# Optimization experiments

Measured on AMD Instinct MI355X. Metric: run time of the kernel, lower is better.

Reference implementation:

```python
import jax, jax.numpy as jnp
import numpy as np

VOCAB, EMBED, HIDDEN, OUT = 1024, 512, 1024, 1024
B, T = 1024, 32


def setup_inputs() -> dict:
    key = jax.random.key(0)
    ks = jax.random.split(key, 10)
    s_emb = 1.0 / np.sqrt(VOCAB)
    s_ih = 1.0 / np.sqrt(HIDDEN)  # PyTorch RNNCell init scale uses hidden_size
    s_out = 1.0 / np.sqrt(HIDDEN)
    return {
        "message": jax.random.normal(ks[0], (B, T, VOCAB), dtype=jnp.float32),
        "W_emb": jax.random.uniform(ks[1], (EMBED, VOCAB), jnp.float32, -s_emb, s_emb),
        "b_emb": jax.random.uniform(ks[2], (EMBED,), jnp.float32, -s_emb, s_emb),
        "W_ih": jax.random.uniform(ks[3], (HIDDEN, EMBED), jnp.float32, -s_ih, s_ih),
        "b_ih": jax.random.uniform(ks[4], (HIDDEN,), jnp.float32, -s_ih, s_ih),
        "W_hh": jax.random.uniform(ks[5], (HIDDEN, HIDDEN), jnp.float32, -s_ih, s_ih),
        "b_hh": jax.random.uniform(ks[6], (HIDDEN,), jnp.float32, -s_ih, s_ih),
        "W_out": jax.random.uniform(ks[7], (OUT, HIDDEN), jnp.float32, -s_out, s_out),
        "b_out": jax.random.uniform(ks[8], (OUT,), jnp.float32, -s_out, s_out),
    }


def reference(message, W_emb, b_emb, W_ih, b_ih, W_hh, b_hh, W_out, b_out):
    # emb: [B, T, E] -- Linear embedding of (relaxed one-hot) message
    emb = jnp.einsum("btv,ev->bte", message, W_emb) + b_emb
    # Precompute input projections for all steps at once: [T, B, H]
    x_proj = jnp.einsum("bte,he->tbh", emb, W_ih) + b_ih

    def step(h, x_t):
        h_new = jnp.tanh(x_t + h @ W_hh.T + b_hh)
        return h_new, None

    h0 = jnp.zeros((message.shape[0], W_hh.shape[0]), dtype=message.dtype)
    h_T, _ = jax.lax.scan(step, h0, x_proj)
    out = h_T @ W_out.T + b_out  # [B, OUT]
    return out  # agent is identity here
```

## Files before the change

### kernel.cpp

```cpp
#include <hip/hip_runtime.h>
#include <cstdint>
#include <cstddef>

#define B_DIM 1024
#define T_DIM 32
#define V_DIM 1024
#define E_DIM 512
#define H_DIM 1024
#define O_DIM 1024

typedef unsigned short u16;
typedef __attribute__((ext_vector_type(8))) __bf16 bf16x8;
typedef __attribute__((ext_vector_type(4))) float f32x4;

__device__ __forceinline__ float bf2f(u16 u) {
  union { unsigned int i; float f; } v; v.i = ((unsigned int)u) << 16; return v.f;
}
__device__ __forceinline__ u16 f2bf(float f) {
  union { float f; unsigned int i; } v; v.f = f;
  return (u16)((v.i + 0x7fffu + ((v.i >> 16) & 1u)) >> 16);
}
__device__ __forceinline__ void async_cp16(const void* g, void* l) {
  __builtin_amdgcn_global_load_lds(
      (const __attribute__((address_space(1))) void*)g,
      (__attribute__((address_space(3))) void*)l, 16, 0, 0);
}
__device__ __forceinline__ float fast_tanh(float v) {
  return 1.f - 2.f / (__expf(2.f * v) + 1.f);
}

__global__ __launch_bounds__(256) void convert_all(
    const float* __restrict__ Whh, const float* __restrict__ Wout,
    const float* __restrict__ msg, u16* __restrict__ dWhh,
    u16* __restrict__ dWout, u16* __restrict__ dmsg) {
  const int QW = 262144;
  const int QM = 8388608;
  const int total = dmsg ? (2 * QW + QM) : (2 * QW);
  int i = blockIdx.x * 256 + threadIdx.x;
  const int stride = gridDim.x * 256;
  for (; i < total; i += stride) {
    const float4* src; ushort4* dst; int j;
    if (i < QW)            { src = (const float4*)Whh;  dst = (ushort4*)dWhh;  j = i; }
    else if (i < 2 * QW)   { src = (const float4*)Wout; dst = (ushort4*)dWout; j = i - QW; }
    else                   { src = (const float4*)msg;  dst = (ushort4*)dmsg;  j = i - 2 * QW; }
    float4 v = src[j];
    ushort4 o = {f2bf(v.x), f2bf(v.y), f2bf(v.z), f2bf(v.w)};
    dst[j] = o;
  }
}

__global__ __launch_bounds__(256) void wcomb_valu(
    const float* __restrict__ Wih, const float* __restrict__ Wemb,
    u16* __restrict__ Wc) {
  __shared__ __align__(16) float As[16][68];
  __shared__ __align__(16) float Bs[16][68];
  const int tx = threadIdx.x & 15, ty = threadIdx.x >> 4;
  const int v0 = blockIdx.x * 64, h0 = blockIdx.y * 64;
  float acc[4][4] = {};
  for (int kt = 0; kt < 32; ++kt) {
#pragma unroll
    for (int i = 0; i < 4; ++i) {
      int idx = threadIdx.x + i * 256;
      int row = idx >> 4, k = idx & 15;
      As[k][row] = Wih[(size_t)(h0 + row) * E_DIM + kt * 16 + k];
      Bs[k][row] = Wemb[(size_t)(kt * 16 + k) * V_DIM + v0 + row];
    }
    __syncthreads();
    for (int k = 0; k < 16; ++k) {
      float4 a = *(const float4*)&As[k][ty * 4];
      float4 b = *(const float4*)&Bs[k][tx * 4];
      const float av[4] = {a.x, a.y, a.z, a.w}, bv[4] = {b.x, b.y, b.z, b.w};
#pragma unroll
      for (int i = 0; i < 4; ++i)
#pragma unroll
        for (int j = 0; j < 4; ++j) acc[i][j] += av[i] * bv[j];
    }
    __syncthreads();
  }
#pragma unroll
  for (int i = 0; i < 4; ++i)
#pragma unroll
    for (int j = 0; j < 4; ++j)
      Wc[(size_t)(h0 + ty * 4 + i) * V_DIM + v0 + tx * 4 + j] = f2bf(acc[i][j]);
}

__global__ __launch_bounds__(256) void bcomb_valu(
    const float* __restrict__ Wih, const float* __restrict__ bemb,
    const float* __restrict__ bih, float* __restrict__ bc) {
  int h = blockIdx.x * 256 + threadIdx.x;
  float s = 0.f;
  for (int e = 0; e < E_DIM; ++e) s += Wih[(size_t)h * E_DIM + e] * bemb[e];
  bc[h] = s + bih[h];
}

template <int MODE>
__global__ __launch_bounds__(256) void gemm_bt(
    const u16* __restrict__ A, const u16* __restrict__ Bm,
    const u16* __restrict__ x, const float* __restrict__ bias,
    void* __restrict__ outp) {
  constexpr int LDSE = 49152;
  __shared__ __align__(16) u16 lds[LDSE];
  const int tid = threadIdx.x, lane = tid & 63, w = tid >> 6;
  const int lrow = lane >> 4, lcol = lane & 15;
  const int l7 = lane & 7, r8 = lane >> 3;
  const int p = blockIdx.x;
  int mt, nt;
  {
    int xk = p & 7, q = p >> 3;
    mt = xk * 32 + (q >> 3);
    nt = q & 7;
  }
  const int m0 = mt * 128, n0 = nt * 128;
  const int mq = (w & 1) * 64, nq = (w >> 1) * 64;
  const int half = w >> 1, wv = w & 1;

  auto stage = [&](int kk, int d) {
    const u16* src = half ? Bm : A;
    const int rbase = half ? n0 : m0;
#pragma unroll
    for (int i = 0; i < 8; ++i) {
      int row = wv * 64 + i * 8 + r8;
      async_cp16(src + (size_t)(rbase + row) * H_DIM + kk * 64 + ((l7 ^ r8) << 3),
                 lds + d * 16384 + half * 8192 + (wv * 64 + i * 8) * 64);
    }
  };

  f32x4 acc[4][4] = {};
  auto kchunk = [&](int d) {
    const u16* base = lds + d * 16384;
#pragma unroll
    for (int ks = 0; ks < 2; ++ks) {
      const int ce = ks * 32 + lrow * 8;
      bf16x8 a[4], b[4];
#pragma unroll
      for (int i = 0; i < 4; ++i) {
        int row = mq + i * 16 + lcol;
        a[i] = *(const bf16x8*)(base + row * 64 + (ce ^ ((row & 7) << 3)));
      }
#pragma unroll
      for (int i = 0; i < 4; ++i) {
        int row = nq + i * 16 + lcol;
        b[i] = *(const bf16x8*)(base + 8192 + row * 64 + (ce ^ ((row & 7) << 3)));
      }
#pragma unroll
      for (int i = 0; i < 4; ++i)
#pragma unroll
        for (int j = 0; j < 4; ++j)
          acc[i][j] = __builtin_amdgcn_mfma_f32_16x16x32_bf16(a[i], b[j], acc[i][j], 0, 0, 0);
    }
  };

  stage(0, 0); stage(1, 1); stage(2, 2);
#pragma unroll
  for (int kk = 0; kk < 16; ++kk) {
    if (kk <= 13)      asm volatile("s_waitcnt vmcnt(16)" ::: "memory");
    else if (kk == 14) asm volatile("s_waitcnt vmcnt(8)" ::: "memory");
    else               asm volatile("s_waitcnt vmcnt(0)" ::: "memory");
    __builtin_amdgcn_s_barrier();
    kchunk(kk % 3);
    __builtin_amdgcn_s_barrier();
    if (kk <= 12) stage(kk + 3, kk % 3);
  }

  float bv[4];
#pragma unroll
  for (int j = 0; j < 4; ++j) bv[j] = bias[n0 + nq + j * 16 + lcol];
#pragma unroll
  for (int i = 0; i < 4; ++i)
#pragma unroll
    for (int rr = 0; rr < 4; ++rr) {
      int rg = m0 + mq + i * 16 + lrow * 4 + rr;
      int bI = rg >> 5, tI = rg & 31;
      u16* dst = (u16*)outp + ((size_t)tI * B_DIM + bI) * H_DIM + n0 + nq;
#pragma unroll
      for (int j = 0; j < 4; ++j)
        dst[j * 16 + lcol] = f2bf(acc[i][j][rr] + bv[j]);
    }
}

template <int MODE>
__global__ __launch_bounds__(256) void step64(
    const u16* __restrict__ A, const u16* __restrict__ Bm,
    const u16* __restrict__ x, const float* __restrict__ bias,
    void* __restrict__ outp) {
  constexpr int XOFF = 24576;
  constexpr int LDSE = (MODE == 1) ? 28672 : 24576;
  __shared__ __align__(16) u16 lds[LDSE];
  const int tid = threadIdx.x, lane = tid & 63, w = tid >> 6;
  const int lrow = lane >> 4, lcol = lane & 15;
  const int l7 = lane & 7, r8 = lane >> 3;
  const int p = blockIdx.x;
  const int xcd = p & 7, q = p >> 3;
  const int mt = xcd * 2 + (q >> 4), nt = q & 15;
  const int m0 = mt * 64, n0 = nt * 64;
  const int mq = (w & 1) * 32, nq = (w >> 1) * 32;
  const int half = w >> 1, wv = w & 1;

  auto stage = [&](int kk, int d) {
    const u16* src = half ? Bm : A;
    const int rbase = half ? n0 : m0;
#pragma unroll
    for (int i = 0; i < 4; ++i) {
      int row = wv * 32 + i * 8 + r8;
      async_cp16(src + (size_t)(rbase + row) * H_DIM + kk * 64 + ((l7 ^ r8) << 3),
                 lds + d * 8192 + half * 4096 + (wv * 32 + i * 8) * 64);
    }
  };
  auto stage_x = [&]() {
#pragma unroll
    for (int i = 0; i < 2; ++i)
      async_cp16(x + (size_t)(m0 + i * 32 + w * 8 + r8) * H_DIM + n0 + l7 * 8,
                 lds + XOFF + (i * 32 + w * 8) * 64);
  };

  f32x4 acc[2][2] = {};
  auto kchunk = [&](int d) {
    const u16* base = lds + d * 8192;
#pragma unroll
    for (int ks = 0; ks < 2; ++ks) {
      const int ce = ks * 32 + lrow * 8;
      bf16x8 a[2], b[2];
#pragma unroll
      for (int i = 0; i < 2; ++i) {
        int row = mq + i * 16 + lcol;
        a[i] = *(const bf16x8*)(base + row * 64 + (ce ^ ((row & 7) << 3)));
      }
#pragma unroll
      for (int j = 0; j < 2; ++j) {
        int row = nq + j * 16 + lcol;
        b[j] = *(const bf16x8*)(base + 4096 + row * 64 + (ce ^ ((row & 7) << 3)));
      }
#pragma unroll
      for (int i = 0; i < 2; ++i)
#pragma unroll
        for (int j = 0; j < 2; ++j)
          acc[i][j] = __builtin_amdgcn_mfma_f32_16x16x32_bf16(a[i], b[j], acc[i][j], 0, 0, 0);
    }
  };

  if (A != nullptr) {
    if (MODE == 1) stage_x();
    stage(0, 0); stage(1, 1); stage(2, 2);
#pragma unroll
    for (int kk = 0; kk < 16; ++kk) {
      if (kk <= 13)      asm volatile("s_waitcnt vmcnt(8)" ::: "memory");
      else if (kk == 14) asm volatile("s_waitcnt vmcnt(4)" ::: "memory");
      else               asm volatile("s_waitcnt vmcnt(0)" ::: "memory");
      __builtin_amdgcn_s_barrier();
      kchunk(kk % 3);
      __builtin_amdgcn_s_barrier();
      if (kk <= 12) stage(kk + 3, kk % 3);
    }
  } else {
    if (MODE == 1) stage_x();
    asm volatile("s_waitcnt vmcnt(0)" ::: "memory");
    __builtin_amdgcn_s_barrier();
  }

  float bv[2] = {bias[n0 + nq + lcol], bias[n0 + nq + 16 + lcol]};
  if (MODE == 2) {
#pragma unroll
    for (int i = 0; i < 2; ++i)
#pragma unroll
      for (int rr = 0; rr < 4; ++rr) {
        int row = m0 + mq + i * 16 + lrow * 4 + rr;
#pragma unroll
        for (int j = 0; j < 2; ++j)
          ((float*)outp)[(size_t)row * O_DIM + n0 + nq + j * 16 + lcol] =
              acc[i][j][rr] + bv[j];
      }
  } else {
#pragma unroll
    for (int i = 0; i < 2; ++i)
#pragma unroll
      for (int rr = 0; rr < 4; ++rr) {
        int rowl = mq + i * 16 + lrow * 4 + rr;
#pragma unroll
        for (int j = 0; j < 2; ++j) {
          int col = nq + j * 16 + lcol;
          float v = acc[i][j][rr] + bv[j] + bf2f(lds[XOFF + rowl * 64 + col]);
          lds[rowl * 64 + col] = f2bf(fast_tanh(v));
        }
      }
    __syncthreads();
    {
      int row = tid >> 2, c = (tid & 3) * 16;
      const uint4* s = (const uint4*)(lds + row * 64 + c);
      uint4 v0 = s[0], v1 = s[1];
      uint4* g = (uint4*)((u16*)outp + (size_t)(m0 + row) * H_DIM + n0 + c);
      g[0] = v0;
      g[1] = v1;
    }
  }
}

__global__ __launch_bounds__(256) void xproj_mfma(
    const float* __restrict__ msg, const u16* __restrict__ Wc,
    const float* __restrict__ bc, u16* __restrict__ xp) {
  __shared__ u16 As[128 * 64];
  __shared__ u16 Bs[128 * 64];
  const int tid = threadIdx.x, lane = tid & 63, w = tid >> 6;
  const int lrow = lane >> 4, lcol = lane & 15;
  const int p = blockIdx.y * gridDim.x + blockIdx.x;
  const int xk = p & 7, q = p >> 3;
  const int m0 = (xk * 32 + (q >> 3)) * 128;
  const int n0 = (q & 7) * 128;
  const int mq = (w & 1) * 64, nq = (w >> 1) * 64;
  f32x4 acc[4][4] = {};
  const int r8 = lane >> 3, l7 = lane & 7;
  const int ar = tid >> 1, ak = (tid & 1) * 32;

  auto stageB = [&](int kk) {
#pragma unroll
    for (int i = 0; i < 4; ++i) {
      int ch = w * 4 + i;
      async_cp16(Wc + (size_t)(n0 + ch * 8 + r8) * V_DIM + kk * 64 + ((l7 ^ r8) << 3),
                 Bs + ch * 512);
    }
  };
  float4 areg[8];
  auto loadA = [&](int kk) {
    const float4* src = (const float4*)(msg + (size_t)(m0 + ar) * V_DIM + kk * 64 + ak);
#pragma unroll
    for (int i = 0; i < 8; ++i) areg[i] = src[i];
  };
  auto writeA = [&]() {
    u16 tmp[32];
#pragma unroll
    for (int i = 0; i < 8; ++i) {
      tmp[i * 4 + 0] = f2bf(areg[i].x);
      tmp[i * 4 + 1] = f2bf(areg[i].y);
      tmp[i * 4 + 2] = f2bf(areg[i].z);
      tmp[i * 4 + 3] = f2bf(areg[i].w);
    }
#pragma unroll
    for (int i = 0; i < 4; ++i) {
      int c = (ak + i * 8) ^ ((ar & 7) << 3);
      *(uint4*)(As + (size_t)ar * 64 + c) = *(const uint4*)(tmp + i * 8);
    }
  };

  loadA(0);
  stageB(0);
  writeA();
  for (int kk = 0; kk < 16; ++kk) {
    __syncthreads();
    if (kk < 15) loadA(kk + 1);
#pragma unroll
    for (int ks = 0; ks < 2; ++ks) {
      const int kb = ks * 32 + lrow * 8;
      bf16x8 a[4], b[4];
#pragma unroll
      for (int i = 0; i < 4; ++i) {
        int row = mq + i * 16 + lcol;
        a[i] = *(const bf16x8*)(As + row * 64 + (kb ^ ((row & 7) << 3)));
      }
#pragma unroll
      for (int i = 0; i < 4; ++i) {
        int row = nq + i * 16 + lcol;
        b[i] = *(const bf16x8*)(Bs + row * 64 + (kb ^ ((row & 7) << 3)));
      }
#pragma unroll
      for (int i = 0; i < 4; ++i)
#pragma unroll
        for (int j = 0; j < 4; ++j)
          acc[i][j] = __builtin_amdgcn_mfma_f32_16x16x32_bf16(a[i], b[j], acc[i][j], 0, 0, 0);
    }
    __syncthreads();
    if (kk < 15) { stageB(kk + 1); writeA(); }
  }
  float bcv[4];
#pragma unroll
  for (int j = 0; j < 4; ++j) bcv[j] = bc[n0 + nq + j * 16 + lcol];
#pragma unroll
  for (int i = 0; i < 4; ++i)
#pragma unroll
    for (int rr = 0; rr < 4; ++rr) {
      int rg = m0 + mq + i * 16 + lrow * 4 + rr;
      int bI = rg >> 5, tI = rg & 31;
      u16* dst = xp + ((size_t)tI * B_DIM + bI) * H_DIM + n0 + nq;
#pragma unroll
      for (int j = 0; j < 4; ++j)
        dst[j * 16 + lcol] = f2bf(acc[i][j][rr] + bcv[j]);
    }
}

extern "C" void kernel_launch(void* const* d_in, const int* in_sizes, int n_in,
                              void* d_out, int out_size, void* d_ws, size_t ws_size,
                              hipStream_t stream) {
  const float* msg  = (const float*)d_in[0];
  const float* Wemb = (const float*)d_in[1];
  const float* bemb = (const float*)d_in[2];
  const float* Wih  = (const float*)d_in[3];
  const float* bih  = (const float*)d_in[4];
  const float* Whh  = (const float*)d_in[5];
  const float* bhh  = (const float*)d_in[6];
  const float* Wout = (const float*)d_in[7];
  const float* bout = (const float*)d_in[8];
  char* ws = (char*)d_ws;

  float* bc   = (float*)ws;
  u16* Wc     = (u16*)(ws + 4096);
  u16* Whh_b  = (u16*)(ws + 2101248);
  u16* Wout_b = (u16*)(ws + 4198400);
  u16* hA     = (u16*)(ws + 6295552);
  u16* hB     = (u16*)(ws + 8392704);
  u16* xp     = (u16*)(ws + 10489856);
  u16* msgb   = (u16*)(ws + 77598720);
  const size_t NEED_SMALL = 77598720;
  const size_t NEED_BIG   = 77598720 + 67108864;
  if (ws_size < NEED_SMALL) return;
  const bool big = ws_size >= NEED_BIG;

  if (big) {
    convert_all<<<2048, 256, 0, stream>>>(Whh, Wout, msg, Whh_b, Wout_b, msgb);
  } else {
    convert_all<<<512, 256, 0, stream>>>(Whh, Wout, nullptr, Whh_b, Wout_b, nullptr);
  }
  wcomb_valu<<<dim3(16, 16), 256, 0, stream>>>(Wih, Wemb, Wc);
  bcomb_valu<<<4, 256, 0, stream>>>(Wih, bemb, bih, bc);

  if (big) {
    gemm_bt<0><<<2048, 256, 0, stream>>>(msgb, Wc, nullptr, bc, xp);
  } else {
    xproj_mfma<<<dim3(8, 256), 256, 0, stream>>>(msg, Wc, bc, xp);
  }

  step64<1><<<256, 256, 0, stream>>>(nullptr, Whh_b, xp, bhh, hA);
  for (int t = 1; t < 32; ++t) {
    const u16* hin = (t & 1) ? hA : hB;
    u16* hout = (t & 1) ? hB : hA;
    step64<1><<<256, 256, 0, stream>>>(hin, Whh_b,
                                       xp + (size_t)t * B_DIM * H_DIM, bhh, hout);
  }
  step64<2><<<256, 256, 0, stream>>>(hB, Wout_b, nullptr, bout, d_out);
}
```

Measured before the change: 566.9 us.

## Replace per-step RNN launches with cooperative kernels using grid-wide atomic barriers

The 32 per-timestep kernel launches become 4 cooperative launches, each running 8 recurrence steps with a grid-wide spin barrier on an atomic counter between steps. Hidden states are written in place over the consumed xp slot, using coherent (sc0 sc1) loads and stores so other blocks see them. The aim is to remove per-launch overhead and tail gaps between steps. The cost is atomic spin-wait synchronization, and correctness depends on all 256 blocks being co-resident.

```diff
diff --git a/kernel.cpp b/kernel.cpp
--- a/kernel.cpp
+++ b/kernel.cpp
@@ -12,6 +12,7 @@
 typedef unsigned short u16;
 typedef __attribute__((ext_vector_type(8))) __bf16 bf16x8;
 typedef __attribute__((ext_vector_type(4))) float f32x4;
+typedef __attribute__((ext_vector_type(4))) unsigned int u32x4;
 
 __device__ __forceinline__ float bf2f(u16 u) {
   union { unsigned int i; float f; } v; v.i = ((unsigned int)u) << 16; return v.f;
@@ -86,30 +87,25 @@
 
 __global__ __launch_bounds__(256) void bcomb_valu(
     const float* __restrict__ Wih, const float* __restrict__ bemb,
-    const float* __restrict__ bih, float* __restrict__ bc) {
+    const float* __restrict__ bih, float* __restrict__ bc,
+    unsigned* __restrict__ ctr) {
+  if (blockIdx.x == 0 && threadIdx.x == 0) *ctr = 0;
   int h = blockIdx.x * 256 + threadIdx.x;
   float s = 0.f;
   for (int e = 0; e < E_DIM; ++e) s += Wih[(size_t)h * E_DIM + e] * bemb[e];
   bc[h] = s + bih[h];
 }
 
-template <int MODE>
-__global__ __launch_bounds__(256) void gemm_bt(
+__global__ __launch_bounds__(256) void gemm_xp(
     const u16* __restrict__ A, const u16* __restrict__ Bm,
-    const u16* __restrict__ x, const float* __restrict__ bias,
-    void* __restrict__ outp) {
-  constexpr int LDSE = 49152;
-  __shared__ __align__(16) u16 lds[LDSE];
+    const float* __restrict__ bias, u16* __restrict__ outp) {
+  __shared__ __align__(16) u16 lds[49152];
   const int tid = threadIdx.x, lane = tid & 63, w = tid >> 6;
   const int lrow = lane >> 4, lcol = lane & 15;
   const int l7 = lane & 7, r8 = lane >> 3;
   const int p = blockIdx.x;
-  int mt, nt;
-  {
-    int xk = p & 7, q = p >> 3;
-    mt = xk * 32 + (q >> 3);
-    nt = q & 7;
-  }
+  const int xk = p & 7, q = p >> 3;
+  const int mt = xk * 32 + (q >> 3), nt = q & 7;
   const int m0 = mt * 128, n0 = nt * 128;
   const int mq = (w & 1) * 64, nq = (w >> 1) * 64;
   const int half = w >> 1, wv = w & 1;
@@ -171,21 +167,17 @@
     for (int rr = 0; rr < 4; ++rr) {
       int rg = m0 + mq + i * 16 + lrow * 4 + rr;
       int bI = rg >> 5, tI = rg & 31;
-      u16* dst = (u16*)outp + ((size_t)tI * B_DIM + bI) * H_DIM + n0 + nq;
+      u16* dst = outp + ((size_t)tI * B_DIM + bI) * H_DIM + n0 + nq;
 #pragma unroll
       for (int j = 0; j < 4; ++j)
         dst[j * 16 + lcol] = f2bf(acc[i][j][rr] + bv[j]);
     }
 }
 
-template <int MODE>
-__global__ __launch_bounds__(256) void step64(
-    const u16* __restrict__ A, const u16* __restrict__ Bm,
-    const u16* __restrict__ x, const float* __restrict__ bias,
-    void* __restrict__ outp) {
-  constexpr int XOFF = 24576;
-  constexpr int LDSE = (MODE == 1) ? 28672 : 24576;
-  __shared__ __align__(16) u16 lds[LDSE];
+__global__ __launch_bounds__(256) void steps8(
+    const u16* __restrict__ Bm, u16* __restrict__ xp,
+    const float* __restrict__ bhh, unsigned* __restrict__ ctr, int t0) {
+  __shared__ __align__(16) u16 lds[24576];
   const int tid = threadIdx.x, lane = tid & 63, w = tid >> 6;
   const int lrow = lane >> 4, lcol = lane & 15;
   const int l7 = lane & 7, r8 = lane >> 3;
@@ -195,6 +187,128 @@
   const int m0 = mt * 64, n0 = nt * 64;
   const int mq = (w & 1) * 32, nq = (w >> 1) * 32;
   const int half = w >> 1, wv = w & 1;
+  const float bv0 = bhh[n0 + nq + lcol], bv1 = bhh[n0 + nq + 16 + lcol];
+  const int xrow = tid >> 2, xce = (tid & 3) * 16;
+
+  for (int s = 0; s < 8; ++s) {
+    const int t = t0 + s;
+    u16* slot = xp + (size_t)t * (B_DIM * H_DIM);
+    const u16* A = (t == 0) ? nullptr : xp + (size_t)(t - 1) * (B_DIM * H_DIM);
+
+    const u16* xgp = slot + (size_t)(m0 + xrow) * H_DIM + n0 + xce;
+    u32x4 xv0, xv1;
+    asm volatile(
+        "global_load_dwordx4 %0, %2, off sc0 sc1\n\t"
+        "global_load_dwordx4 %1, %3, off sc0 sc1"
+        : "=v"(xv0), "=v"(xv1)
+        : "v"(xgp), "v"(xgp + 8)
+        : "memory");
+
+    f32x4 acc[2][2] = {};
+    if (A != nullptr) {
+      auto stage = [&](int kk, int d) {
+        const u16* src = half ? Bm : A;
+        const int rbase = half ? n0 : m0;
+#pragma unroll
+        for (int i = 0; i < 4; ++i) {
+          int row = wv * 32 + i * 8 + r8;
+          async_cp16(src + (size_t)(rbase + row) * H_DIM + kk * 64 + ((l7 ^ r8) << 3),
+                     lds + d * 8192 + half * 4096 + (wv * 32 + i * 8) * 64);
+        }
+      };
+      stage(0, 0); stage(1, 1); stage(2, 2);
+#pragma unroll
+      for (int kk = 0; kk < 16; ++kk) {
+        if (kk <= 13)      asm volatile("s_waitcnt vmcnt(8)" ::: "memory");
+        else if (kk == 14) asm volatile("s_waitcnt vmcnt(4)" ::: "memory");
+        else               asm volatile("s_waitcnt vmcnt(0)" ::: "memory");
+        __builtin_amdgcn_s_barrier();
+        {
+          const u16* base = lds + (kk % 3) * 8192;
+#pragma unroll
+          for (int ks = 0; ks < 2; ++ks) {
+            const int ce = ks * 32 + lrow * 8;
+            bf16x8 a0, a1, b0, b1;
+            {
+              int rA0 = mq + lcol, rA1 = mq + 16 + lcol;
+              int rB0 = nq + lcol, rB1 = nq + 16 + lcol;
+              a0 = *(const bf16x8*)(base + rA0 * 64 + (ce ^ ((rA0 & 7) << 3)));
+              a1 = *(const bf16x8*)(base + rA1 * 64 + (ce ^ ((rA1 & 7) << 3)));
+              b0 = *(const bf16x8*)(base + 4096 + rB0 * 64 + (ce ^ ((rB0 & 7) << 3)));
+              b1 = *(const bf16x8*)(base + 4096 + rB1 * 64 + (ce ^ ((rB1 & 7) << 3)));
+            }
+            acc[0][0] = __builtin_amdgcn_mfma_f32_16x16x32_bf16(a0, b0, acc[0][0], 0, 0, 0);
+            acc[0][1] = __builtin_amdgcn_mfma_f32_16x16x32_bf16(a0, b1, acc[0][1], 0, 0, 0);
+            acc[1][0] = __builtin_amdgcn_mfma_f32_16x16x32_bf16(a1, b0, acc[1][0], 0, 0, 0);
+            acc[1][1] = __builtin_amdgcn_mfma_f32_16x16x32_bf16(a1, b1, acc[1][1], 0, 0, 0);
+          }
+        }
+        __builtin_amdgcn_s_barrier();
+        if (kk <= 12) stage(kk + 3, kk % 3);
+      }
+    } else {
+      asm volatile("s_waitcnt vmcnt(0)" ::: "memory");
+      __builtin_amdgcn_s_barrier();
+    }
+
+    *(u32x4*)(lds + 8192 + xrow * 64 + xce) = xv0;
+    *(u32x4*)(lds + 8192 + xrow * 64 + xce + 8) = xv1;
+    __syncthreads();
+#pragma unroll
+    for (int i = 0; i < 2; ++i)
+#pragma unroll
+      for (int rr = 0; rr < 4; ++rr) {
+        int rowl = mq + i * 16 + lrow * 4 + rr;
+#pragma unroll
+        for (int j = 0; j < 2; ++j) {
+          int col = nq + j * 16 + lcol;
+          float v = acc[i][j][rr] + (j ? bv1 : bv0) + bf2f(lds[8192 + rowl * 64 + col]);
+          lds[rowl * 64 + col] = f2bf(fast_tanh(v));
+        }
+      }
+    __syncthreads();
+    {
+      const u32x4* sp = (const u32x4*)(lds + xrow * 64 + xce);
+      u32x4 h0 = sp[0], h1 = sp[1];
+      u16* gp = slot + (size_t)(m0 + xrow) * H_DIM + n0 + xce;
+      if (s < 7) {
+        asm volatile(
+            "global_store_dwordx4 %0, %2, off sc0 sc1\n\t"
+            "global_store_dwordx4 %1, %3, off sc0 sc1"
+            :: "v"(gp), "v"(gp + 8), "v"(h0), "v"(h1)
+            : "memory");
+        asm volatile("s_waitcnt vmcnt(0)" ::: "memory");
+        __syncthreads();
+        if (tid == 0) {
+          const unsigned tgt = 256u * (unsigned)(7 * (t0 >> 3) + s + 1);
+          __hip_atomic_fetch_add(ctr, 1u, __ATOMIC_RELAXED,
+                                 __HIP_MEMORY_SCOPE_AGENT);
+          while (__hip_atomic_load(ctr, __ATOMIC_RELAXED,
+                                   __HIP_MEMORY_SCOPE_AGENT) < tgt)
+            __builtin_amdgcn_s_sleep(4);
+        }
+        __syncthreads();
+      } else {
+        *(u32x4*)gp = h0;
+        *(u32x4*)(gp + 8) = h1;
+      }
+    }
+  }
+}
+
+__global__ __launch_bounds__(256) void out_gemm(
+    const u16* __restrict__ A, const u16* __restrict__ Bm,
+    const float* __restrict__ bias, float* __restrict__ outp) {
+  __shared__ __align__(16) u16 lds[24576];
+  const int tid = threadIdx.x, lane = tid & 63, w = tid >> 6;
+  const int lrow = lane >> 4, lcol = lane & 15;
+  const int l7 = lane & 7, r8 = lane >> 3;
+  const int p = blockIdx.x;
+  const int xcd = p & 7, q = p >> 3;
+  const int mt = xcd * 2 + (q >> 4), nt = q & 15;
+  const int m0 = mt * 64, n0 = nt * 64;
+  const int mq = (w & 1) * 32, nq = (w >> 1) * 32;
+  const int half = w >> 1, wv = w & 1;
 
   auto stage = [&](int kk, int d) {
     const u16* src = half ? Bm : A;
@@ -206,92 +320,46 @@
                  lds + d * 8192 + half * 4096 + (wv * 32 + i * 8) * 64);
     }
   };
-  auto stage_x = [&]() {
-#pragma unroll
-    for (int i = 0; i < 2; ++i)
-      async_cp16(x + (size_t)(m0 + i * 32 + w * 8 + r8) * H_DIM + n0 + l7 * 8,
-                 lds + XOFF + (i * 32 + w * 8) * 64);
-  };
-
   f32x4 acc[2][2] = {};
   auto kchunk = [&](int d) {
     const u16* base = lds + d * 8192;
 #pragma unroll
     for (int ks = 0; ks < 2; ++ks) {
       const int ce = ks * 32 + lrow * 8;
-      bf16x8 a[2], b[2];
-#pragma unroll
-      for (int i = 0; i < 2; ++i) {
-        int row = mq + i * 16 + lcol;
-        a[i] = *(const bf16x8*)(base + row * 64 + (ce ^ ((row & 7) << 3)));
-      }
-#pragma unroll
-      for (int j = 0; j < 2; ++j) {
-        int row = nq + j * 16 + lcol;
-        b[j] = *(const bf16x8*)(base + 4096 + row * 64 + (ce ^ ((row & 7) << 3)));
-      }
-#pragma unroll
-      for (int i = 0; i < 2; ++i)
-#pragma unroll
-        for (int j = 0; j < 2; ++j)
-          acc[i][j] = __builtin_amdgcn_mfma_f32_16x16x32_bf16(a[i], b[j], acc[i][j], 0, 0, 0);
-    }
-  };
-
-  if (A != nullptr) {
-    if (MODE == 1) stage_x();
-    stage(0, 0); stage(1, 1); stage(2, 2);
-#pragma unroll
-    for (int kk = 0; kk < 16; ++kk) {
-      if (kk <= 13)      asm volatile("s_waitcnt vmcnt(8)" ::: "memory");
-      else if (kk == 14) asm volatile("s_waitcnt vmcnt(4)" ::: "memory");
-      else               asm volatile("s_waitcnt vmcnt(0)" ::: "memory");
-      __builtin_amdgcn_s_barrier();
-      kchunk(kk % 3);
-      __builtin_amdgcn_s_barrier();
-      if (kk <= 12) stage(kk + 3, kk % 3);
-    }
-  } else {
-    if (MODE == 1) stage_x();
-    asm volatile("s_waitcnt vmcnt(0)" ::: "memory");
+      int rA0 = mq + lcol, rA1 = mq + 16 + lcol;
+      int rB0 = nq + lcol, rB1 = nq + 16 + lcol;
+      bf16x8 a0 = *(const bf16x8*)(base + rA0 * 64 + (ce ^ ((rA0 & 7) << 3)));
+      bf16x8 a1 = *(const bf16x8*)(base + rA1 * 64 + (ce ^ ((rA1 & 7) << 3)));
+      bf16x8 b0 = *(const bf16x8*)(base + 4096 + rB0 * 64 + (ce ^ ((rB0 & 7) << 3)));
+      bf16x8 b1 = *(const bf16x8*)(base + 4096 + rB1 * 64 + (ce ^ ((rB1 & 7) << 3)));
+      acc[0][0] = __builtin_amdgcn_mfma_f32_16x16x32_bf16(a0, b0, acc[0][0], 0, 0, 0);
+      acc[0][1] = __builtin_amdgcn_mfma_f32_16x16x32_bf16(a0, b1, acc[0][1], 0, 0, 0);
+      acc[1][0] = __builtin_amdgcn_mfma_f32_16x16x32_bf16(a1, b0, acc[1][0], 0, 0, 0);
+      acc[1][1] = __builtin_amdgcn_mfma_f32_16x16x32_bf16(a1, b1, acc[1][1], 0, 0, 0);
+    }
+  };
+  stage(0, 0); stage(1, 1); stage(2, 2);
+#pragma unroll
+  for (int kk = 0; kk < 16; ++kk) {
+    if (kk <= 13)      asm volatile("s_waitcnt vmcnt(8)" ::: "memory");
+    else if (kk == 14) asm volatile("s_waitcnt vmcnt(4)" ::: "memory");
+    else               asm volatile("s_waitcnt vmcnt(0)" ::: "memory");
     __builtin_amdgcn_s_barrier();
-  }
-
+    kchunk(kk % 3);
+    __builtin_amdgcn_s_barrier();
+    if (kk <= 12) stage(kk + 3, kk % 3);
+  }
   float bv[2] = {bias[n0 + nq + lcol], bias[n0 + nq + 16 + lcol]};
-  if (MODE == 2) {
-#pragma unroll
-    for (int i = 0; i < 2; ++i)
-#pragma unroll
-      for (int rr = 0; rr < 4; ++rr) {
-        int row = m0 + mq + i * 16 + lrow * 4 + rr;
-#pragma unroll
-        for (int j = 0; j < 2; ++j)
-          ((float*)outp)[(size_t)row * O_DIM + n0 + nq + j * 16 + lcol] =
-              acc[i][j][rr] + bv[j];
-      }
-  } else {
-#pragma unroll
-    for (int i = 0; i < 2; ++i)
-#pragma unroll
-      for (int rr = 0; rr < 4; ++rr) {
-        int rowl = mq + i * 16 + lrow * 4 + rr;
-#pragma unroll
-        for (int j = 0; j < 2; ++j) {
-          int col = nq + j * 16 + lcol;
-          float v = acc[i][j][rr] + bv[j] + bf2f(lds[XOFF + rowl * 64 + col]);
-          lds[rowl * 64 + col] = f2bf(fast_tanh(v));
-        }
-      }
-    __syncthreads();
-    {
-      int row = tid >> 2, c = (tid & 3) * 16;
-      const uint4* s = (const uint4*)(lds + row * 64 + c);
-      uint4 v0 = s[0], v1 = s[1];
-      uint4* g = (uint4*)((u16*)outp + (size_t)(m0 + row) * H_DIM + n0 + c);
-      g[0] = v0;
-      g[1] = v1;
-    }
-  }
+#pragma unroll
+  for (int i = 0; i < 2; ++i)
+#pragma unroll
+    for (int rr = 0; rr < 4; ++rr) {
+      int row = m0 + mq + i * 16 + lrow * 4 + rr;
+#pragma unroll
+      for (int j = 0; j < 2; ++j)
+        outp[(size_t)row * O_DIM + n0 + nq + j * 16 + lcol] =
+            acc[i][j][rr] + bv[j];
+    }
 }
 
 __global__ __launch_bounds__(256) void xproj_mfma(
@@ -399,14 +467,13 @@
   const float* bout = (const float*)d_in[8];
   char* ws = (char*)d_ws;
 
-  float* bc   = (float*)ws;
-  u16* Wc     = (u16*)(ws + 4096);
-  u16* Whh_b  = (u16*)(ws + 2101248);
-  u16* Wout_b = (u16*)(ws + 4198400);
-  u16* hA     = (u16*)(ws + 6295552);
-  u16* hB     = (u16*)(ws + 8392704);
-  u16* xp     = (u16*)(ws + 10489856);
-  u16* msgb   = (u16*)(ws + 77598720);
+  float* bc     = (float*)ws;
+  u16* Wc       = (u16*)(ws + 4096);
+  u16* Whh_b    = (u16*)(ws + 2101248);
+  u16* Wout_b   = (u16*)(ws + 4198400);
+  unsigned* ctr = (unsigned*)(ws + 6295552);
+  u16* xp       = (u16*)(ws + 10489856);
+  u16* msgb     = (u16*)(ws + 77598720);
   const size_t NEED_SMALL = 77598720;
   const size_t NEED_BIG   = 77598720 + 67108864;
   if (ws_size < NEED_SMALL) return;
@@ -418,20 +485,22 @@
     convert_all<<<512, 256, 0, stream>>>(Whh, Wout, nullptr, Whh_b, Wout_b, nullptr);
   }
   wcomb_valu<<<dim3(16, 16), 256, 0, stream>>>(Wih, Wemb, Wc);
-  bcomb_valu<<<4, 256, 0, stream>>>(Wih, bemb, bih, bc);
+  bcomb_valu<<<4, 256, 0, stream>>>(Wih, bemb, bih, bc, ctr);
 
   if (big) {
-    gemm_bt<0><<<2048, 256, 0, stream>>>(msgb, Wc, nullptr, bc, xp);
+    gemm_xp<<<2048, 256, 0, stream>>>(msgb, Wc, bc, xp);
   } else {
     xproj_mfma<<<dim3(8, 256), 256, 0, stream>>>(msg, Wc, bc, xp);
   }
 
-  step64<1><<<256, 256, 0, stream>>>(nullptr, Whh_b, xp, bhh, hA);
-  for (int t = 1; t < 32; ++t) {
-    const u16* hin = (t & 1) ? hA : hB;
-    u16* hout = (t & 1) ? hB : hA;
-    step64<1><<<256, 256, 0, stream>>>(hin, Whh_b,
-                                       xp + (size_t)t * B_DIM * H_DIM, bhh, hout);
-  }
-  step64<2><<<256, 256, 0, stream>>>(hB, Wout_b, nullptr, bout, d_out);
-}
+  for (int c = 0; c < 4; ++c) {
+    const u16* a_w = Whh_b; u16* a_xp = xp; const float* a_b = bhh;
+    unsigned* a_c = ctr; int a_t0 = c * 8;
+    void* kargs[] = {(void*)&a_w, (void*)&a_xp, (void*)&a_b,
+                     (void*)&a_c, (void*)&a_t0};
+    (void)hipLaunchCooperativeKernel((const void*)steps8, dim3(256), dim3(256),
+                                     kargs, 0, stream);
+  }
+  out_gemm<<<256, 256, 0, stream>>>(xp + (size_t)31 * B_DIM * H_DIM, Wout_b,
+                                    bout, (float*)d_out);
+}
```

Result: slower. 773.8 us (+36.5%).

## Fuse prep kernels, fold first RNN step into xproj GEMM, double-buffer

Applied to the files above, without the earlier changes.

Merges the weight conversion, combined-weight GEMM and combined-bias kernels into one launch that dispatches on block index. The x-projection GEMM epilogue now applies tanh with b_hh for t=0, since h0 is zero, which removes one recurrent step launch. The GEMM's LDS pipeline drops from triple to double buffering, which cuts LDS use but gives less latency hiding. The fused prep kernel puts light and heavy work under a single grid, and the first step now writes its h output into the xp buffer.

```diff
diff --git a/kernel.cpp b/kernel.cpp
--- a/kernel.cpp
+++ b/kernel.cpp
@@ -29,87 +29,80 @@
   return 1.f - 2.f / (__expf(2.f * v) + 1.f);
 }
 
-__global__ __launch_bounds__(256) void convert_all(
+__global__ __launch_bounds__(256) void prep_all(
     const float* __restrict__ Whh, const float* __restrict__ Wout,
-    const float* __restrict__ msg, u16* __restrict__ dWhh,
-    u16* __restrict__ dWout, u16* __restrict__ dmsg) {
-  const int QW = 262144;
-  const int QM = 8388608;
-  const int total = dmsg ? (2 * QW + QM) : (2 * QW);
-  int i = blockIdx.x * 256 + threadIdx.x;
-  const int stride = gridDim.x * 256;
-  for (; i < total; i += stride) {
-    const float4* src; ushort4* dst; int j;
-    if (i < QW)            { src = (const float4*)Whh;  dst = (ushort4*)dWhh;  j = i; }
-    else if (i < 2 * QW)   { src = (const float4*)Wout; dst = (ushort4*)dWout; j = i - QW; }
-    else                   { src = (const float4*)msg;  dst = (ushort4*)dmsg;  j = i - 2 * QW; }
-    float4 v = src[j];
-    ushort4 o = {f2bf(v.x), f2bf(v.y), f2bf(v.z), f2bf(v.w)};
-    dst[j] = o;
-  }
-}
-
-__global__ __launch_bounds__(256) void wcomb_valu(
-    const float* __restrict__ Wih, const float* __restrict__ Wemb,
-    u16* __restrict__ Wc) {
+    const float* __restrict__ msg, const float* __restrict__ Wih,
+    const float* __restrict__ Wemb, const float* __restrict__ bemb,
+    const float* __restrict__ bih, u16* __restrict__ dWhh,
+    u16* __restrict__ dWout, u16* __restrict__ dmsg,
+    u16* __restrict__ Wc, float* __restrict__ bc) {
   __shared__ __align__(16) float As[16][68];
   __shared__ __align__(16) float Bs[16][68];
-  const int tx = threadIdx.x & 15, ty = threadIdx.x >> 4;
-  const int v0 = blockIdx.x * 64, h0 = blockIdx.y * 64;
-  float acc[4][4] = {};
-  for (int kt = 0; kt < 32; ++kt) {
-#pragma unroll
-    for (int i = 0; i < 4; ++i) {
-      int idx = threadIdx.x + i * 256;
-      int row = idx >> 4, k = idx & 15;
-      As[k][row] = Wih[(size_t)(h0 + row) * E_DIM + kt * 16 + k];
-      Bs[k][row] = Wemb[(size_t)(kt * 16 + k) * V_DIM + v0 + row];
-    }
-    __syncthreads();
-    for (int k = 0; k < 16; ++k) {
-      float4 a = *(const float4*)&As[k][ty * 4];
-      float4 b = *(const float4*)&Bs[k][tx * 4];
-      const float av[4] = {a.x, a.y, a.z, a.w}, bv[4] = {b.x, b.y, b.z, b.w};
-#pragma unroll
-      for (int i = 0; i < 4; ++i)
-#pragma unroll
-        for (int j = 0; j < 4; ++j) acc[i][j] += av[i] * bv[j];
-    }
-    __syncthreads();
-  }
-#pragma unroll
-  for (int i = 0; i < 4; ++i)
-#pragma unroll
-    for (int j = 0; j < 4; ++j)
-      Wc[(size_t)(h0 + ty * 4 + i) * V_DIM + v0 + tx * 4 + j] = f2bf(acc[i][j]);
-}
-
-__global__ __launch_bounds__(256) void bcomb_valu(
-    const float* __restrict__ Wih, const float* __restrict__ bemb,
-    const float* __restrict__ bih, float* __restrict__ bc) {
-  int h = blockIdx.x * 256 + threadIdx.x;
-  float s = 0.f;
-  for (int e = 0; e < E_DIM; ++e) s += Wih[(size_t)h * E_DIM + e] * bemb[e];
-  bc[h] = s + bih[h];
-}
-
-template <int MODE>
-__global__ __launch_bounds__(256) void gemm_bt(
+  const int bid = blockIdx.x;
+  if (bid < 2048) {
+    const int QW = 262144;
+    const int QM = 8388608;
+    const int total = dmsg ? (2 * QW + QM) : (2 * QW);
+    int i = bid * 256 + threadIdx.x;
+    const int stride = 2048 * 256;
+    for (; i < total; i += stride) {
+      const float4* src; ushort4* dst; int j;
+      if (i < QW)          { src = (const float4*)Whh;  dst = (ushort4*)dWhh;  j = i; }
+      else if (i < 2 * QW) { src = (const float4*)Wout; dst = (ushort4*)dWout; j = i - QW; }
+      else                 { src = (const float4*)msg;  dst = (ushort4*)dmsg;  j = i - 2 * QW; }
+      float4 v = src[j];
+      ushort4 o = {f2bf(v.x), f2bf(v.y), f2bf(v.z), f2bf(v.w)};
+      dst[j] = o;
+    }
+  } else if (bid < 2304) {
+    const int b2 = bid - 2048;
+    const int tx = threadIdx.x & 15, ty = threadIdx.x >> 4;
+    const int v0 = (b2 & 15) * 64, h0 = (b2 >> 4) * 64;
+    float acc[4][4] = {};
+    for (int kt = 0; kt < 32; ++kt) {
+#pragma unroll
+      for (int i = 0; i < 4; ++i) {
+        int idx = threadIdx.x + i * 256;
+        int row = idx >> 4, k = idx & 15;
+        As[k][row] = Wih[(size_t)(h0 + row) * E_DIM + kt * 16 + k];
+        Bs[k][row] = Wemb[(size_t)(kt * 16 + k) * V_DIM + v0 + row];
+      }
+      __syncthreads();
+      for (int k = 0; k < 16; ++k) {
+        float4 a = *(const float4*)&As[k][ty * 4];
+        float4 b = *(const float4*)&Bs[k][tx * 4];
+        const float av[4] = {a.x, a.y, a.z, a.w}, bv[4] = {b.x, b.y, b.z, b.w};
+#pragma unroll
+        for (int i = 0; i < 4; ++i)
+#pragma unroll
+          for (int j = 0; j < 4; ++j) acc[i][j] += av[i] * bv[j];
+      }
+      __syncthreads();
+    }
+#pragma unroll
+    for (int i = 0; i < 4; ++i)
+#pragma unroll
+      for (int j = 0; j < 4; ++j)
+        Wc[(size_t)(h0 + ty * 4 + i) * V_DIM + v0 + tx * 4 + j] = f2bf(acc[i][j]);
+  } else {
+    int h = (bid - 2304) * 256 + threadIdx.x;
+    float s = 0.f;
+    for (int e = 0; e < E_DIM; ++e) s += Wih[(size_t)h * E_DIM + e] * bemb[e];
+    bc[h] = s + bih[h];
+  }
+}
+
+__global__ __launch_bounds__(256) void gemm_xp(
     const u16* __restrict__ A, const u16* __restrict__ Bm,
-    const u16* __restrict__ x, const float* __restrict__ bias,
-    void* __restrict__ outp) {
-  constexpr int LDSE = 49152;
-  __shared__ __align__(16) u16 lds[LDSE];
+    const float* __restrict__ bias, const float* __restrict__ bhh,
+    u16* __restrict__ outp) {
+  __shared__ __align__(16) u16 lds[32768];
   const int tid = threadIdx.x, lane = tid & 63, w = tid >> 6;
   const int lrow = lane >> 4, lcol = lane & 15;
   const int l7 = lane & 7, r8 = lane >> 3;
   const int p = blockIdx.x;
-  int mt, nt;
-  {
-    int xk = p & 7, q = p >> 3;
-    mt = xk * 32 + (q >> 3);
-    nt = q & 7;
-  }
+  const int xk = p & 7, q = p >> 3;
+  const int mt = xk * 32 + (q >> 3), nt = q & 7;
   const int m0 = mt * 128, n0 = nt * 128;
   const int mq = (w & 1) * 64, nq = (w >> 1) * 64;
   const int half = w >> 1, wv = w & 1;
@@ -150,31 +143,39 @@
     }
   };
 
-  stage(0, 0); stage(1, 1); stage(2, 2);
+  stage(0, 0); stage(1, 1);
 #pragma unroll
   for (int kk = 0; kk < 16; ++kk) {
-    if (kk <= 13)      asm volatile("s_waitcnt vmcnt(16)" ::: "memory");
-    else if (kk == 14) asm volatile("s_waitcnt vmcnt(8)" ::: "memory");
-    else               asm volatile("s_waitcnt vmcnt(0)" ::: "memory");
+    if (kk <= 14) asm volatile("s_waitcnt vmcnt(8)" ::: "memory");
+    else          asm volatile("s_waitcnt vmcnt(0)" ::: "memory");
     __builtin_amdgcn_s_barrier();
-    kchunk(kk % 3);
+    kchunk(kk & 1);
     __builtin_amdgcn_s_barrier();
-    if (kk <= 12) stage(kk + 3, kk % 3);
-  }
-
-  float bv[4];
-#pragma unroll
-  for (int j = 0; j < 4; ++j) bv[j] = bias[n0 + nq + j * 16 + lcol];
+    if (kk <= 13) stage(kk + 2, kk & 1);
+  }
+
+  float bv[4], bh[4];
+#pragma unroll
+  for (int j = 0; j < 4; ++j) {
+    bv[j] = bias[n0 + nq + j * 16 + lcol];
+    bh[j] = bhh[n0 + nq + j * 16 + lcol];
+  }
 #pragma unroll
   for (int i = 0; i < 4; ++i)
 #pragma unroll
     for (int rr = 0; rr < 4; ++rr) {
       int rg = m0 + mq + i * 16 + lrow * 4 + rr;
       int bI = rg >> 5, tI = rg & 31;
-      u16* dst = (u16*)outp + ((size_t)tI * B_DIM + bI) * H_DIM + n0 + nq;
-#pragma unroll
-      for (int j = 0; j < 4; ++j)
-        dst[j * 16 + lcol] = f2bf(acc[i][j][rr] + bv[j]);
+      u16* dst = outp + ((size_t)tI * B_DIM + bI) * H_DIM + n0 + nq;
+      if (tI == 0) {
+#pragma unroll
+        for (int j = 0; j < 4; ++j)
+          dst[j * 16 + lcol] = f2bf(fast_tanh(acc[i][j][rr] + bv[j] + bh[j]));
+      } else {
+#pragma unroll
+        for (int j = 0; j < 4; ++j)
+          dst[j * 16 + lcol] = f2bf(acc[i][j][rr] + bv[j]);
+      }
     }
 }
 
@@ -412,26 +413,29 @@
   if (ws_size < NEED_SMALL) return;
   const bool big = ws_size >= NEED_BIG;
 
+  prep_all<<<2308, 256, 0, stream>>>(Whh, Wout, big ? msg : nullptr, Wih, Wemb,
+                                     bemb, bih, Whh_b, Wout_b,
+                                     big ? msgb : nullptr, Wc, bc);
+
   if (big) {
-    convert_all<<<2048, 256, 0, stream>>>(Whh, Wout, msg, Whh_b, Wout_b, msgb);
-  } else {
-    convert_all<<<512, 256, 0, stream>>>(Whh, Wout, nullptr, Whh_b, Wout_b, nullptr);
-  }
-  wcomb_valu<<<dim3(16, 16), 256, 0, stream>>>(Wih, Wemb, Wc);
-  bcomb_valu<<<4, 256, 0, stream>>>(Wih, bemb, bih, bc);
-
-  if (big) {
-    gemm_bt<0><<<2048, 256, 0, stream>>>(msgb, Wc, nullptr, bc, xp);
+    gemm_xp<<<2048, 256, 0, stream>>>(msgb, Wc, bc, bhh, xp);
+    step64<1><<<256, 256, 0, stream>>>(xp, Whh_b,
+                                       xp + (size_t)1 * B_DIM * H_DIM, bhh, hB);
+    for (int t = 2; t < 32; ++t) {
+      const u16* hin = (t & 1) ? hA : hB;
+      u16* hout = (t & 1) ? hB : hA;
+      step64<1><<<256, 256, 0, stream>>>(hin, Whh_b,
+                                         xp + (size_t)t * B_DIM * H_DIM, bhh, hout);
+    }
   } else {
     xproj_mfma<<<dim3(8, 256), 256, 0, stream>>>(msg, Wc, bc, xp);
-  }
-
-  step64<1><<<256, 256, 0, stream>>>(nullptr, Whh_b, xp, bhh, hA);
-  for (int t = 1; t < 32; ++t) {
-    const u16* hin = (t & 1) ? hA : hB;
-    u16* hout = (t & 1) ? hB : hA;
-    step64<1><<<256, 256, 0, stream>>>(hin, Whh_b,
-                                       xp + (size_t)t * B_DIM * H_DIM, bhh, hout);
+    step64<1><<<256, 256, 0, stream>>>(nullptr, Whh_b, xp, bhh, hA);
+    for (int t = 1; t < 32; ++t) {
+      const u16* hin = (t & 1) ? hA : hB;
+      u16* hout = (t & 1) ? hB : hA;
+      step64<1><<<256, 256, 0, stream>>>(hin, Whh_b,
+                                         xp + (size_t)t * B_DIM * H_DIM, bhh, hout);
+    }
   }
   step64<2><<<256, 256, 0, stream>>>(hB, Wout_b, nullptr, bout, d_out);
 }
```

Measured after the change: 546.8 us. -3.5%, faster.
